# Optimization experiments

Hardware: AMD Instinct MI355X
Metric: run time of the kernel (lower is better)

## Reference

```python
import jax, jax.numpy as jnp
import numpy as np

B, N, D, K = 32, 4096, 128, 512
NPB = 2048          # unique tail nodes per batch (>= K so topk branch is taken)
M = B * NPB         # total unique tail nodes
E = B * N           # total edges
NUM_ENT = 10000


def setup_inputs() -> dict:
    key = jax.random.key(0)
    ks = jax.random.split(key, 18)
    f = lambda k, s: jax.random.normal(k, s, dtype=jnp.float32)
    inp = {
        "q_head": f(ks[0], (B, D)),
        "q_rel": f(ks[1], (B, D)),
        "q_time": f(ks[2], (B, D)),
        "r_neighbor": f(ks[3], (B, N, D)),
        "t_neighbor": f(ks[4], (B, N, D)),
        "time_neighbor": f(ks[5], (B, N, D)),
        "hidden": f(ks[6], (E, D)),
        "tail_emd": jnp.zeros((M, D), jnp.float32),  # scatter out-buffer
    }
    # tail_index: each edge of batch b scatters into that batch's node slab
    local = jax.random.randint(ks[7], (B, N), 0, NPB)
    inp["tail_index"] = (local + jnp.arange(B)[:, None] * NPB).reshape(E).astype(jnp.int32)
    # tail_nodes: [M,3] = (batch id, tail entity, time)
    batch_col = jnp.repeat(jnp.arange(B), NPB)
    tail_col = jax.random.randint(ks[8], (M,), 0, NUM_ENT)
    time_col = jax.random.randint(ks[9], (M,), 0, 365)
    inp["tail_nodes"] = jnp.stack([batch_col, tail_col, time_col], axis=-1).astype(jnp.int32)
    # linear-layer params (torch nn.Linear-style scaling)
    s3, s1 = 1.0 / np.sqrt(3 * D), 1.0 / np.sqrt(D)
    inp["W_q"] = f(ks[10], (3 * D, D)) * s3
    inp["b_q"] = jnp.zeros((D,), jnp.float32)
    inp["W_a"] = f(ks[11], (3 * D, D)) * s3
    inp["b_a"] = jnp.zeros((D,), jnp.float32)
    inp["W_att"] = f(ks[12], (3 * D, 1)) * s3
    inp["b_att"] = jnp.zeros((1,), jnp.float32)
    inp["W_rule"] = f(ks[13], (D, 1)) * s1
    inp["b_rule"] = jnp.zeros((1,), jnp.float32)
    inp["W_out"] = f(ks[14], (D, D)) * s1
    inp["b_out"] = jnp.zeros((D,), jnp.float32)
    return inp


def reference(q_head, q_rel, q_time, r_neighbor, t_neighbor, time_neighbor,
              hidden, tail_emd, tail_index, tail_nodes,
              W_q, b_q, W_a, b_a, W_att, b_att, W_rule, b_rule, W_out, b_out):
    # act = identity (module default). reduce = 'sum'.
    # raw message per edge: [E, D]
    message = (q_head[:, None, :] + r_neighbor + time_neighbor).reshape(E, D)
    # query / neighbor projections
    query = jnp.concatenate([q_head, q_rel, q_time], axis=-1) @ W_q + b_q      # [B, D]
    neigh = jnp.concatenate([r_neighbor, t_neighbor, time_neighbor], -1) @ W_a + b_a  # [B, N, D]
    q = query[:, None, :]
    qa = jnp.concatenate([q * neigh, q - neigh, q + neigh], axis=-1)           # [B, N, 3D]
    att1 = jax.nn.sigmoid(qa @ W_att + b_att).reshape(E, 1)
    att2 = jax.nn.sigmoid(hidden @ W_rule + b_rule)                            # [E, 1]
    att = (att1 + att2) * 0.5
    msg = att * message
    # scatter-sum aggregation over unique tail nodes
    seg = lambda v: jax.ops.segment_sum(v, tail_index, num_segments=M)
    tail_agg = tail_emd + seg(msg)            # scatter(..., out=tail_emd)
    new_hidden = seg(hidden)                  # [M, D]
    agg_att = seg(att[:, 0])                  # [M]
    # per-batch top-k over aggregated attention (each batch has NPB >= K nodes)
    nodes_batch = tail_nodes[:, 0]
    scores = jnp.where(nodes_batch[None, :] == jnp.arange(B)[:, None],
                       agg_att[None, :], -jnp.inf)                             # [B, M]
    _, idx = jax.lax.top_k(scores, K)                                          # [B, K] global node ids
    new_nodes = jnp.stack([tail_nodes[:, 1][idx], tail_nodes[:, 2][idx]], -1)  # [B, K, 2]
    emd = tail_agg[idx]                                                        # [B, K, D]
    hid = new_hidden[idx]                                                      # [B, K, D]
    out_emd = emd @ W_out + b_out                                              # act=identity
    return new_nodes, out_emd, hid
```

## Files before the change

### kernel.cpp

```cpp
#include <hip/hip_runtime.h>
#include <math.h>

#define B 32
#define N 4096
#define D 128
#define KTOP 512
#define NPB 2048
#define MSEG (B * NPB)
#define E (B * N)
#define MAXC 32
#define K7ROWS 16

__global__ __launch_bounds__(128) void k0_precompute(
    const float* __restrict__ qh, const float* __restrict__ qr,
    const float* __restrict__ qt, const float* __restrict__ Wq,
    const float* __restrict__ bq, const float* __restrict__ Wa,
    const float* __restrict__ ba, const float* __restrict__ Watt,
    const float* __restrict__ batt, float* __restrict__ vf,
    float* __restrict__ c2f) {
  int b = blockIdx.x, d = threadIdx.x;
  __shared__ double u[128];
  __shared__ double red[128];
  const float* qhb = qh + b * 128;
  const float* qrb = qr + b * 128;
  const float* qtb = qt + b * 128;
  double a0 = 0, a1 = 0, a2 = 0, a3 = 0;
#pragma unroll 4
  for (int i = 0; i < 128; i += 4) {
    a0 += (double)qhb[i] * (double)Wq[i * 128 + d];
    a1 += (double)qhb[i + 1] * (double)Wq[(i + 1) * 128 + d];
    a2 += (double)qhb[i + 2] * (double)Wq[(i + 2) * 128 + d];
    a3 += (double)qhb[i + 3] * (double)Wq[(i + 3) * 128 + d];
  }
#pragma unroll 4
  for (int i = 0; i < 128; i += 4) {
    a0 += (double)qrb[i] * (double)Wq[(128 + i) * 128 + d];
    a1 += (double)qrb[i + 1] * (double)Wq[(129 + i) * 128 + d];
    a2 += (double)qrb[i + 2] * (double)Wq[(130 + i) * 128 + d];
    a3 += (double)qrb[i + 3] * (double)Wq[(131 + i) * 128 + d];
  }
#pragma unroll 4
  for (int i = 0; i < 128; i += 4) {
    a0 += (double)qtb[i] * (double)Wq[(256 + i) * 128 + d];
    a1 += (double)qtb[i + 1] * (double)Wq[(257 + i) * 128 + d];
    a2 += (double)qtb[i + 2] * (double)Wq[(258 + i) * 128 + d];
    a3 += (double)qtb[i + 3] * (double)Wq[(259 + i) * 128 + d];
  }
  double acc = (double)bq[d] + ((a0 + a1) + (a2 + a3));
  double w1 = (double)Watt[d], w2 = (double)Watt[128 + d], w3 = (double)Watt[256 + d];
  double ud = acc * w1 - w2 + w3;
  u[d] = ud;
  red[d] = acc * (w2 + w3) + (double)ba[d] * ud;
  __syncthreads();
  for (int s = 64; s > 0; s >>= 1) {
    if (d < s) red[d] += red[d + s];
    __syncthreads();
  }
  if (d == 0) c2f[b] = (float)(red[0] + (double)batt[0]);
  for (int i = d; i < 384; i += 128) {
    double v0 = 0, v1 = 0, v2 = 0, v3 = 0;
#pragma unroll 4
    for (int dd = 0; dd < 128; dd += 4) {
      v0 += (double)Wa[i * 128 + dd] * u[dd];
      v1 += (double)Wa[i * 128 + dd + 1] * u[dd + 1];
      v2 += (double)Wa[i * 128 + dd + 2] * u[dd + 2];
      v3 += (double)Wa[i * 128 + dd + 3] * u[dd + 3];
    }
    vf[b * 384 + i] = (float)((v0 + v1) + (v2 + v3));
  }
}

__global__ __launch_bounds__(256) void k1_att(
    const float* __restrict__ r, const float* __restrict__ t,
    const float* __restrict__ tm, const float* __restrict__ hidden,
    const float* __restrict__ Wrule, const float* __restrict__ brule,
    const float* __restrict__ vf, const float* __restrict__ c2f,
    const int* __restrict__ tidx, float* __restrict__ attw,
    double* __restrict__ aggd) {
  int tid = threadIdx.x;
  int h = tid >> 5;
  int l = tid & 31;
  int base = blockIdx.x * 64;
  int b = base >> 12;
  const float4* vb = (const float4*)(vf + b * 384);
  float4 v0 = vb[l];
  float4 v1 = vb[32 + l];
  float4 v2 = vb[64 + l];
  float4 wr = ((const float4*)Wrule)[l];
  float c2 = c2f[b];
  float br = brule[0];
#pragma unroll 4
  for (int i = 0; i < 8; ++i) {
    int e = base + i * 8 + h;
    size_t eo = (size_t)e * 128 + l * 4;
    float4 ra = *(const float4*)(r + eo);
    float4 ta = *(const float4*)(t + eo);
    float4 ma = *(const float4*)(tm + eo);
    float4 ha = *(const float4*)(hidden + eo);
    float p1 = ra.x * v0.x + ra.y * v0.y + ra.z * v0.z + ra.w * v0.w;
    p1 += ta.x * v1.x + ta.y * v1.y + ta.z * v1.z + ta.w * v1.w;
    p1 += ma.x * v2.x + ma.y * v2.y + ma.z * v2.z + ma.w * v2.w;
    float p2 = ha.x * wr.x + ha.y * wr.y + ha.z * wr.z + ha.w * wr.w;
#pragma unroll
    for (int off = 16; off > 0; off >>= 1) {
      p1 += __shfl_xor(p1, off);
      p2 += __shfl_xor(p2, off);
    }
    if (l == 0) {
      float a1 = 1.0f / (1.0f + expf(-(p1 + c2)));
      float a2 = 1.0f / (1.0f + expf(-(p2 + br)));
      float a = 0.5f * (a1 + a2);
      attw[e] = a;
      atomicAdd(&aggd[tidx[e]], (double)a);
    }
  }
}

__global__ __launch_bounds__(256) void kb_build(const int* __restrict__ tidx,
                                                int* __restrict__ counts,
                                                int* __restrict__ lists) {
  int e = blockIdx.x * 256 + threadIdx.x;
  int m = tidx[e];
  int pos = atomicAdd(&counts[m], 1);
  if (pos < MAXC) lists[m * MAXC + pos] = e;
}

__global__ __launch_bounds__(256) void k6_topk(
    const double* __restrict__ aggd, const int* __restrict__ tail_nodes,
    float* __restrict__ out_nodes, int* __restrict__ idxw) {
  __shared__ double sv[2048];
  int b = blockIdx.x >> 3;
  int chunk = blockIdx.x & 7;
  int tid = threadIdx.x;
  for (int s = tid; s < 2048; s += 256) sv[s] = aggd[b * 2048 + s];
  __syncthreads();
  int i = chunk * 256 + tid;
  double vi = sv[i];
  int rank = 0;
#pragma unroll 8
  for (int j = 0; j < 2048; ++j) {
    double vj = sv[j];
    rank += (vj > vi) || (vj == vi && j < i);
  }
  if (rank < KTOP) {
    int gm = b * 2048 + i;
    int p = b * KTOP + rank;
    out_nodes[p * 2 + 0] = (float)tail_nodes[gm * 3 + 1];
    out_nodes[p * 2 + 1] = (float)tail_nodes[gm * 3 + 2];
    idxw[p] = gm;
  }
}

__global__ __launch_bounds__(256) void k7_out(
    const float* __restrict__ tail_emd, const float* __restrict__ r,
    const float* __restrict__ tm, const float* __restrict__ hidden,
    const float* __restrict__ qh, const float* __restrict__ attw,
    const int* __restrict__ counts, const int* __restrict__ lists,
    const float* __restrict__ Wout, const float* __restrict__ bout,
    const int* __restrict__ idxw, float* __restrict__ out_emd,
    float* __restrict__ out_hid) {
  __shared__ float es[K7ROWS][128];
  int tid = threadIdx.x;
  int sub = tid >> 7, d = tid & 127;
  int base = blockIdx.x * K7ROWS;
  for (int j = 0; j < K7ROWS; j += 2) {
    int row = base + j + sub;
    int m = idxw[row];
    int b = m >> 11;
    int cnt = counts[m];
    if (cnt > MAXC) cnt = MAXC;
    float accT = tail_emd[(size_t)m * 128 + d];
    float accH = 0.f;
    float qhd = qh[b * 128 + d];
    for (int jj = 0; jj < cnt; ++jj) {
      int e = lists[m * MAXC + jj];
      float a = attw[e];
      size_t eo = (size_t)e * 128 + d;
      accT += a * (qhd + r[eo] + tm[eo]);
      accH += hidden[eo];
    }
    es[j + sub][d] = accT;
    out_hid[(size_t)row * 128 + d] = accH;
  }
  __syncthreads();
  int cg = tid & 31;
  int rg = tid >> 5;
  float4 bo = *(const float4*)(bout + cg * 4);
  float acc0x = bo.x, acc0y = bo.y, acc0z = bo.z, acc0w = bo.w;
  float acc1x = bo.x, acc1y = bo.y, acc1z = bo.z, acc1w = bo.w;
#pragma unroll 4
  for (int i = 0; i < 128; ++i) {
    float4 w = *(const float4*)(Wout + i * 128 + cg * 4);
    float e0 = es[rg * 2 + 0][i];
    float e1 = es[rg * 2 + 1][i];
    acc0x += e0 * w.x; acc0y += e0 * w.y; acc0z += e0 * w.z; acc0w += e0 * w.w;
    acc1x += e1 * w.x; acc1y += e1 * w.y; acc1z += e1 * w.z; acc1w += e1 * w.w;
  }
  size_t r0 = (size_t)(base + rg * 2) * 128 + cg * 4;
  *(float4*)(out_emd + r0) = make_float4(acc0x, acc0y, acc0z, acc0w);
  *(float4*)(out_emd + r0 + 128) = make_float4(acc1x, acc1y, acc1z, acc1w);
}

extern "C" void kernel_launch(void* const* d_in, const int* in_sizes, int n_in,
                              void* d_out, int out_size, void* d_ws,
                              size_t ws_size, hipStream_t stream) {
  const float* q_head = (const float*)d_in[0];
  const float* q_rel = (const float*)d_in[1];
  const float* q_time = (const float*)d_in[2];
  const float* r_nb = (const float*)d_in[3];
  const float* t_nb = (const float*)d_in[4];
  const float* tm_nb = (const float*)d_in[5];
  const float* hidden = (const float*)d_in[6];
  const float* tail_emd = (const float*)d_in[7];
  const int* tail_index = (const int*)d_in[8];
  const int* tail_nodes = (const int*)d_in[9];
  const float* W_q = (const float*)d_in[10];
  const float* b_q = (const float*)d_in[11];
  const float* W_a = (const float*)d_in[12];
  const float* b_a = (const float*)d_in[13];
  const float* W_att = (const float*)d_in[14];
  const float* b_att = (const float*)d_in[15];
  const float* W_rule = (const float*)d_in[16];
  const float* b_rule = (const float*)d_in[17];
  const float* W_out = (const float*)d_in[18];
  const float* b_out = (const float*)d_in[19];

  char* ws = (char*)d_ws;
  float* vf = (float*)(ws + 0);
  float* c2f = (float*)(ws + 49152);
  float* attw = (float*)(ws + 49280);
  int* counts = (int*)(ws + 573568);
  int* lists = (int*)(ws + 835712);
  double* aggd = (double*)(ws + 9224320);
  int* idxw = (int*)(ws + 9748608);

  float* out_nodes = (float*)d_out;
  float* out_emd = (float*)d_out + (size_t)B * KTOP * 2;
  float* out_hid = out_emd + (size_t)B * KTOP * 128;

  hipMemsetAsync(counts, 0, MSEG * sizeof(int), stream);
  hipMemsetAsync(aggd, 0, MSEG * sizeof(double), stream);
  k0_precompute<<<B, 128, 0, stream>>>(q_head, q_rel, q_time, W_q, b_q, W_a,
                                       b_a, W_att, b_att, vf, c2f);
  k1_att<<<E / 64, 256, 0, stream>>>(r_nb, t_nb, tm_nb, hidden, W_rule, b_rule,
                                     vf, c2f, tail_index, attw, aggd);
  kb_build<<<E / 256, 256, 0, stream>>>(tail_index, counts, lists);
  k6_topk<<<B * 8, 256, 0, stream>>>(aggd, tail_nodes, out_nodes, idxw);
  k7_out<<<(B * KTOP) / K7ROWS, 256, 0, stream>>>(tail_emd, r_nb, tm_nb,
                                                  hidden, q_head, attw, counts,
                                                  lists, W_out, b_out, idxw,
                                                  out_emd, out_hid);
}
```

Baseline: 461.9 us.

## Fuse list building into attention kernel and vectorize gather and top-k loops

Folds the per-node edge list construction into the attention kernel, so a separate pass over the tail indices and one launch are removed. The two memsets are merged into one by placing counts and aggd next to each other in the workspace. The attention kernel is remapped to four threads per edge with weights staged in shared memory, and the k7 gather uses float4 loads with a padded shared tile. The top-k rank loop reads pairs of doubles. Because lists are now filled in attention-kernel order, edge order inside each list can change, which changes float summation order slightly.

```diff
diff --git a/kernel.cpp b/kernel.cpp
--- a/kernel.cpp
+++ b/kernel.cpp
@@ -76,53 +76,56 @@
     const float* __restrict__ Wrule, const float* __restrict__ brule,
     const float* __restrict__ vf, const float* __restrict__ c2f,
     const int* __restrict__ tidx, float* __restrict__ attw,
-    double* __restrict__ aggd) {
+    double* __restrict__ aggd, int* __restrict__ counts,
+    int* __restrict__ lists) {
+  __shared__ float sAll[512];
   int tid = threadIdx.x;
-  int h = tid >> 5;
-  int l = tid & 31;
   int base = blockIdx.x * 64;
   int b = base >> 12;
-  const float4* vb = (const float4*)(vf + b * 384);
-  float4 v0 = vb[l];
-  float4 v1 = vb[32 + l];
-  float4 v2 = vb[64 + l];
-  float4 wr = ((const float4*)Wrule)[l];
-  float c2 = c2f[b];
-  float br = brule[0];
-#pragma unroll 4
+  for (int i = tid; i < 512; i += 256)
+    sAll[i] = (i < 384) ? vf[b * 384 + i] : Wrule[i - 384];
+  __syncthreads();
+  int q = tid & 3;
+  int e = base + (tid >> 2);
+  float4 acc1 = make_float4(0.f, 0.f, 0.f, 0.f);
+  float4 acc2 = make_float4(0.f, 0.f, 0.f, 0.f);
+  size_t erow = (size_t)e * 128;
+#pragma unroll
   for (int i = 0; i < 8; ++i) {
-    int e = base + i * 8 + h;
-    size_t eo = (size_t)e * 128 + l * 4;
-    float4 ra = *(const float4*)(r + eo);
-    float4 ta = *(const float4*)(t + eo);
-    float4 ma = *(const float4*)(tm + eo);
-    float4 ha = *(const float4*)(hidden + eo);
-    float p1 = ra.x * v0.x + ra.y * v0.y + ra.z * v0.z + ra.w * v0.w;
-    p1 += ta.x * v1.x + ta.y * v1.y + ta.z * v1.z + ta.w * v1.w;
-    p1 += ma.x * v2.x + ma.y * v2.y + ma.z * v2.z + ma.w * v2.w;
-    float p2 = ha.x * wr.x + ha.y * wr.y + ha.z * wr.z + ha.w * wr.w;
-#pragma unroll
-    for (int off = 16; off > 0; off >>= 1) {
-      p1 += __shfl_xor(p1, off);
-      p2 += __shfl_xor(p2, off);
-    }
-    if (l == 0) {
-      float a1 = 1.0f / (1.0f + expf(-(p1 + c2)));
-      float a2 = 1.0f / (1.0f + expf(-(p2 + br)));
-      float a = 0.5f * (a1 + a2);
-      attw[e] = a;
-      atomicAdd(&aggd[tidx[e]], (double)a);
-    }
-  }
-}
-
-__global__ __launch_bounds__(256) void kb_build(const int* __restrict__ tidx,
-                                                int* __restrict__ counts,
-                                                int* __restrict__ lists) {
-  int e = blockIdx.x * 256 + threadIdx.x;
-  int m = tidx[e];
-  int pos = atomicAdd(&counts[m], 1);
-  if (pos < MAXC) lists[m * MAXC + pos] = e;
+    int co = i * 16 + q * 4;
+    float4 v0 = *(const float4*)&sAll[co];
+    float4 v1 = *(const float4*)&sAll[128 + co];
+    float4 v2 = *(const float4*)&sAll[256 + co];
+    float4 w4 = *(const float4*)&sAll[384 + co];
+    float4 ra = *(const float4*)(r + erow + co);
+    float4 ta = *(const float4*)(t + erow + co);
+    float4 ma = *(const float4*)(tm + erow + co);
+    float4 ha = *(const float4*)(hidden + erow + co);
+    acc1.x += ra.x * v0.x + ta.x * v1.x + ma.x * v2.x;
+    acc1.y += ra.y * v0.y + ta.y * v1.y + ma.y * v2.y;
+    acc1.z += ra.z * v0.z + ta.z * v1.z + ma.z * v2.z;
+    acc1.w += ra.w * v0.w + ta.w * v1.w + ma.w * v2.w;
+    acc2.x += ha.x * w4.x;
+    acc2.y += ha.y * w4.y;
+    acc2.z += ha.z * w4.z;
+    acc2.w += ha.w * w4.w;
+  }
+  float p1 = (acc1.x + acc1.y) + (acc1.z + acc1.w);
+  float p2 = (acc2.x + acc2.y) + (acc2.z + acc2.w);
+  p1 += __shfl_xor(p1, 1);
+  p2 += __shfl_xor(p2, 1);
+  p1 += __shfl_xor(p1, 2);
+  p2 += __shfl_xor(p2, 2);
+  if (q == 0) {
+    float a1 = 1.0f / (1.0f + expf(-(p1 + c2f[b])));
+    float a2 = 1.0f / (1.0f + expf(-(p2 + brule[0])));
+    float a = 0.5f * (a1 + a2);
+    attw[e] = a;
+    int m = tidx[e];
+    atomicAdd(&aggd[m], (double)a);
+    int pos = atomicAdd(&counts[m], 1);
+    if (pos < MAXC) lists[m * MAXC + pos] = e;
+  }
 }
 
 __global__ __launch_bounds__(256) void k6_topk(
@@ -136,11 +139,13 @@
   __syncthreads();
   int i = chunk * 256 + tid;
   double vi = sv[i];
+  const double2* sv2 = (const double2*)sv;
   int rank = 0;
-#pragma unroll 8
-  for (int j = 0; j < 2048; ++j) {
-    double vj = sv[j];
-    rank += (vj > vi) || (vj == vi && j < i);
+#pragma unroll 4
+  for (int j2 = 0; j2 < 1024; ++j2) {
+    double2 vv = sv2[j2];
+    rank += (vv.x > vi) || (vv.x == vi && (2 * j2) < i);
+    rank += (vv.y > vi) || (vv.y == vi && (2 * j2 + 1) < i);
   }
   if (rank < KTOP) {
     int gm = b * 2048 + i;
@@ -159,28 +164,36 @@
     const float* __restrict__ Wout, const float* __restrict__ bout,
     const int* __restrict__ idxw, float* __restrict__ out_emd,
     float* __restrict__ out_hid) {
-  __shared__ float es[K7ROWS][128];
+  __shared__ float es[K7ROWS][132];
   int tid = threadIdx.x;
-  int sub = tid >> 7, d = tid & 127;
+  int r0 = tid >> 5;
+  int l = tid & 31;
   int base = blockIdx.x * K7ROWS;
-  for (int j = 0; j < K7ROWS; j += 2) {
-    int row = base + j + sub;
+#pragma unroll
+  for (int p = 0; p < 2; ++p) {
+    int row = base + p * 8 + r0;
     int m = idxw[row];
-    int b = m >> 11;
+    int bb = m >> 11;
     int cnt = counts[m];
     if (cnt > MAXC) cnt = MAXC;
-    float accT = tail_emd[(size_t)m * 128 + d];
-    float accH = 0.f;
-    float qhd = qh[b * 128 + d];
+    float4 accT = *(const float4*)(tail_emd + (size_t)m * 128 + l * 4);
+    float4 qh4 = *(const float4*)(qh + bb * 128 + l * 4);
+    float4 accH = make_float4(0.f, 0.f, 0.f, 0.f);
     for (int jj = 0; jj < cnt; ++jj) {
       int e = lists[m * MAXC + jj];
       float a = attw[e];
-      size_t eo = (size_t)e * 128 + d;
-      accT += a * (qhd + r[eo] + tm[eo]);
-      accH += hidden[eo];
+      size_t eo = (size_t)e * 128 + l * 4;
+      float4 ra = *(const float4*)(r + eo);
+      float4 ma = *(const float4*)(tm + eo);
+      float4 ha = *(const float4*)(hidden + eo);
+      accT.x += a * (qh4.x + ra.x + ma.x);
+      accT.y += a * (qh4.y + ra.y + ma.y);
+      accT.z += a * (qh4.z + ra.z + ma.z);
+      accT.w += a * (qh4.w + ra.w + ma.w);
+      accH.x += ha.x; accH.y += ha.y; accH.z += ha.z; accH.w += ha.w;
     }
-    es[j + sub][d] = accT;
-    out_hid[(size_t)row * 128 + d] = accH;
+    *(float4*)&es[p * 8 + r0][l * 4] = accT;
+    *(float4*)(out_hid + (size_t)row * 128 + l * 4) = accH;
   }
   __syncthreads();
   int cg = tid & 31;
@@ -196,9 +209,9 @@
     acc0x += e0 * w.x; acc0y += e0 * w.y; acc0z += e0 * w.z; acc0w += e0 * w.w;
     acc1x += e1 * w.x; acc1y += e1 * w.y; acc1z += e1 * w.z; acc1w += e1 * w.w;
   }
-  size_t r0 = (size_t)(base + rg * 2) * 128 + cg * 4;
-  *(float4*)(out_emd + r0) = make_float4(acc0x, acc0y, acc0z, acc0w);
-  *(float4*)(out_emd + r0 + 128) = make_float4(acc1x, acc1y, acc1z, acc1w);
+  size_t o0 = (size_t)(base + rg * 2) * 128 + cg * 4;
+  *(float4*)(out_emd + o0) = make_float4(acc0x, acc0y, acc0z, acc0w);
+  *(float4*)(out_emd + o0 + 128) = make_float4(acc1x, acc1y, acc1z, acc1w);
 }
 
 extern "C" void kernel_launch(void* const* d_in, const int* in_sizes, int n_in,
@@ -226,25 +239,24 @@
   const float* b_out = (const float*)d_in[19];
 
   char* ws = (char*)d_ws;
-  float* vf = (float*)(ws + 0);
-  float* c2f = (float*)(ws + 49152);
-  float* attw = (float*)(ws + 49280);
-  int* counts = (int*)(ws + 573568);
-  int* lists = (int*)(ws + 835712);
-  double* aggd = (double*)(ws + 9224320);
+  int* counts = (int*)(ws + 0);
+  double* aggd = (double*)(ws + 262144);
+  float* vf = (float*)(ws + 786432);
+  float* c2f = (float*)(ws + 835584);
+  float* attw = (float*)(ws + 835712);
+  int* lists = (int*)(ws + 1360000);
   int* idxw = (int*)(ws + 9748608);
 
   float* out_nodes = (float*)d_out;
   float* out_emd = (float*)d_out + (size_t)B * KTOP * 2;
   float* out_hid = out_emd + (size_t)B * KTOP * 128;
 
-  hipMemsetAsync(counts, 0, MSEG * sizeof(int), stream);
-  hipMemsetAsync(aggd, 0, MSEG * sizeof(double), stream);
+  hipMemsetAsync(counts, 0, 786432, stream);
   k0_precompute<<<B, 128, 0, stream>>>(q_head, q_rel, q_time, W_q, b_q, W_a,
                                        b_a, W_att, b_att, vf, c2f);
   k1_att<<<E / 64, 256, 0, stream>>>(r_nb, t_nb, tm_nb, hidden, W_rule, b_rule,
-                                     vf, c2f, tail_index, attw, aggd);
-  kb_build<<<E / 256, 256, 0, stream>>>(tail_index, counts, lists);
+                                     vf, c2f, tail_index, attw, aggd, counts,
+                                     lists);
   k6_topk<<<B * 8, 256, 0, stream>>>(aggd, tail_nodes, out_nodes, idxw);
   k7_out<<<(B * KTOP) / K7ROWS, 256, 0, stream>>>(tail_emd, r_nb, tm_nb,
                                                   hidden, q_head, attw, counts,
```

Result: slower. 486.2 us (+5.3%).
